# Kernel tuning notes

Measured on AMD Instinct MI355X. Metric: run time of the kernel, lower is better.

The kernel has to match this reference:

```python
import jax, jax.numpy as jnp
import numpy as np

N, IN_DIM, UNITS, Z_DEPTH, Z_K = 8192, 1024, 512, 32, 256


def setup_inputs() -> dict:
    key = jax.random.key(0)
    ks = jax.random.split(key, 10)
    s = 0.02
    return {
        "x": jax.random.normal(ks[0], (N, IN_DIM), jnp.float32),
        "h_W": jax.random.normal(ks[1], (IN_DIM, UNITS), jnp.float32) * s,
        "h_U": jax.random.normal(ks[2], (UNITS, UNITS), jnp.float32) * s,
        "h_b": jnp.zeros((UNITS,), jnp.float32),
        "f_W": jax.random.normal(ks[3], (UNITS, UNITS), jnp.float32) * s,
        "f_b": jnp.zeros((UNITS,), jnp.float32),
        "i_W": jax.random.normal(ks[4], (UNITS, UNITS), jnp.float32) * s,
        "i_b": jnp.zeros((UNITS,), jnp.float32),
        "c_W": jax.random.normal(ks[5], (UNITS, UNITS), jnp.float32) * s,
        "c_b": jnp.zeros((UNITS,), jnp.float32),
        "o_W": jax.random.normal(ks[6], (UNITS, UNITS), jnp.float32) * s,
        "o_b": jnp.zeros((UNITS,), jnp.float32),
        "t_W": jax.random.normal(ks[7], (UNITS, UNITS), jnp.float32) * s,
        "t_b": jnp.zeros((UNITS,), jnp.float32),
        "y_W": jax.random.normal(ks[8], (UNITS, Z_K), jnp.float32) * s,
        "y_b": jnp.zeros((Z_K,), jnp.float32),
        "h0": jnp.zeros((1, UNITS), jnp.float32),
        "z_depth": Z_DEPTH,
    }


def reference(x, h_W, h_U, h_b, f_W, f_b, i_W, i_b, c_W, c_b, o_W, o_b,
              t_W, t_b, y_W, y_b, h0, z_depth):
    n = x.shape[0]
    # x @ h_W is the same every step; hoist it out of the scan.
    xh = x @ h_W + h_b  # [n, units]

    def step(h_prev, _):
        h = jnp.tanh(xh + h_prev @ h_U)
        f = jax.nn.sigmoid(h @ f_W + f_b)
        i = jax.nn.sigmoid(h @ i_W + i_b)
        c = jnp.tanh(h @ c_W + c_b)
        o = jax.nn.sigmoid(h @ o_W + o_b)
        h1 = h_prev * f + c * i
        t = jnp.tanh((o * h1) @ t_W + t_b)
        y = jnp.tanh(t @ y_W + y_b)  # activation=tanh
        return h1, y

    h_init = jnp.broadcast_to(h0, (n, h0.shape[1]))
    _, ys = jax.lax.scan(step, h_init, None, length=z_depth)  # ys: [z_depth, n, z_k]
    return jnp.transpose(ys, (1, 0, 2))  # [n, z_depth, z_k]
```

## Files before the change

### kernel.cpp

```cpp
#include <hip/hip_runtime.h>


typedef _Float16 half_t;
typedef _Float16 half8 __attribute__((ext_vector_type(8)));
typedef _Float16 half4v __attribute__((ext_vector_type(4)));
typedef float float4_ __attribute__((ext_vector_type(4)));

#define UNITS 512
#define IN_DIM 1024
#define NROWS 8192
#define DEPTH 32
#define ZK 256
#define MT 32
#define PITCH (UNITS + 8)
#define XPITCH (IN_DIM + 8)

__device__ inline float4_ mfma16(half8 a, half8 b, float4_ c) {
  return __builtin_amdgcn_mfma_f32_16x16x32_f16(a, b, c, 0, 0, 0);
}
__device__ inline float fast_sigmoid(float x) {
  return __builtin_amdgcn_rcpf(1.0f + __builtin_amdgcn_exp2f(-1.4426950408889634f * x));
}
__device__ inline float fast_tanh(float x) {
  return 2.0f * __builtin_amdgcn_rcpf(1.0f + __builtin_amdgcn_exp2f(-2.8853900817779268f * x)) - 1.0f;
}

template<int NM, class OffF>
__device__ inline void sweepW(const half_t* __restrict__ wbase, OffF off,
                              const half_t* __restrict__ abase,
                              float4_ (&acc)[NM][2]) {
#pragma unroll
  for (int i = 0; i < NM; ++i) {
    acc[i][0] = {0.f, 0.f, 0.f, 0.f};
    acc[i][1] = {0.f, 0.f, 0.f, 0.f};
  }
  half8 w0[2][NM], w1[2][NM];
#pragma unroll
  for (int i = 0; i < NM; ++i) {
    w0[0][i] = *(const half8*)(wbase + off(i));
    w1[0][i] = *(const half8*)(wbase + off(i) + 32);
  }
#pragma unroll
  for (int kk = 0; kk < 8; ++kk) {
    const int cur = kk & 1, nxt = cur ^ 1;
    const int knext = ((kk + 1) & 7) * 64;
#pragma unroll
    for (int i = 0; i < NM; ++i) {
      w0[nxt][i] = *(const half8*)(wbase + off(i) + knext);
      w1[nxt][i] = *(const half8*)(wbase + off(i) + knext + 32);
    }
    const int k0 = kk * 64;
    half8 a00 = *(const half8*)(abase + k0);
    half8 a01 = *(const half8*)(abase + k0 + 32);
    half8 a10 = *(const half8*)(abase + 16 * PITCH + k0);
    half8 a11 = *(const half8*)(abase + 16 * PITCH + k0 + 32);
#pragma unroll
    for (int i = 0; i < NM; ++i) {
      acc[i][0] = mfma16(w0[cur][i], a00, acc[i][0]);
      acc[i][0] = mfma16(w1[cur][i], a01, acc[i][0]);
      acc[i][1] = mfma16(w0[cur][i], a10, acc[i][1]);
      acc[i][1] = mfma16(w1[cur][i], a11, acc[i][1]);
    }
  }
}

template<int NB, int K, int AP, class OffF>
__device__ inline void stage_gemm(const half_t* __restrict__ bbase, OffF off,
                                  const half_t* __restrict__ A, int q, int c16,
                                  float4_ (&acc)[NB][2]) {
#pragma unroll
  for (int nb = 0; nb < NB; ++nb) {
    acc[nb][0] = {0.f, 0.f, 0.f, 0.f};
    acc[nb][1] = {0.f, 0.f, 0.f, 0.f};
  }
  for (int k0 = 0; k0 < K; k0 += 64) {
    const half_t* ap = A + c16 * AP + k0 + q * 8;
    half8 a00 = *(const half8*)(ap);
    half8 a01 = *(const half8*)(ap + 32);
    half8 a10 = *(const half8*)(ap + 16 * AP);
    half8 a11 = *(const half8*)(ap + 16 * AP + 32);
#pragma unroll
    for (int nb = 0; nb < NB; ++nb) {
      const half_t* bp = bbase + off(nb) + k0;
      half8 b0 = *(const half8*)(bp);
      half8 b1 = *(const half8*)(bp + 32);
      acc[nb][0] = mfma16(a00, b0, acc[nb][0]);
      acc[nb][0] = mfma16(a01, b1, acc[nb][0]);
      acc[nb][1] = mfma16(a10, b0, acc[nb][1]);
      acc[nb][1] = mfma16(a11, b1, acc[nb][1]);
    }
  }
}

__global__ void transpose_convert(const float* __restrict__ in, half_t* __restrict__ out,
                                  int R, int C) {
  __shared__ float tile[32][33];
  int c0 = blockIdx.x * 32, r0 = blockIdx.y * 32;
  int tx = threadIdx.x, ty = threadIdx.y;
#pragma unroll
  for (int i = 0; i < 32; i += 8)
    tile[ty + i][tx] = in[(size_t)(r0 + ty + i) * C + c0 + tx];
  __syncthreads();
#pragma unroll
  for (int i = 0; i < 32; i += 8)
    out[(size_t)(c0 + ty + i) * R + r0 + tx] = (half_t)tile[tx][ty + i];
}

__global__ __launch_bounds__(512, 2) void xh_kernel(
    const float* __restrict__ x, const half_t* __restrict__ hW_T,
    const float* __restrict__ h_b, half_t* __restrict__ xh_g) {
  extern __shared__ half_t sx[];
  const int tid = threadIdx.x;
  const int w = tid >> 6, l = tid & 63, q = l >> 4, c16 = l & 15;
  const int row0 = blockIdx.x * 32;
  for (int it = tid; it < 32 * IN_DIM / 4; it += 512) {
    int r = it >> 8;
    int c = (it & 255) * 4;
    float4_ v = __builtin_nontemporal_load((const float4_*)(x + (size_t)(row0 + r) * IN_DIM + c));
    half4v hv;
    hv[0] = (half_t)v[0]; hv[1] = (half_t)v[1]; hv[2] = (half_t)v[2]; hv[3] = (half_t)v[3];
    *(half4v*)(sx + r * XPITCH + c) = hv;
  }
  __syncthreads();
  const int n0 = w * 64;
  float4_ acc[4][2];
  const half_t* bbase = hW_T + (size_t)(n0 + c16) * IN_DIM + q * 8;
  stage_gemm<4, IN_DIM, XPITCH>(bbase, [](int nb) { return nb * 16 * IN_DIM; }, sx, q, c16, acc);
#pragma unroll
  for (int nb = 0; nb < 4; ++nb)
#pragma unroll
    for (int mb = 0; mb < 2; ++mb)
#pragma unroll
      for (int r = 0; r < 4; ++r) {
        int row = mb * 16 + q * 4 + r;
        int col = n0 + nb * 16 + c16;
        xh_g[(size_t)(row0 + row) * UNITS + col] = (half_t)(acc[nb][mb][r] + h_b[col]);
      }
}

__global__ __launch_bounds__(512, 2) void lstm_main(
    const half_t* __restrict__ xh_g, const half_t* __restrict__ hU_T,
    const half_t* __restrict__ W4_T, const half_t* __restrict__ tW_T,
    const half_t* __restrict__ yW_T,
    const float* __restrict__ f_b, const float* __restrict__ i_b,
    const float* __restrict__ c_b, const float* __restrict__ o_b,
    const float* __restrict__ t_b, const float* __restrict__ y_b,
    const float* __restrict__ h0, float* __restrict__ out) {
  extern __shared__ half_t smem[];
  half_t* bufA = smem;
  half_t* bufB = smem + MT * PITCH;
  half_t* s_xh = smem + 2 * MT * PITCH;
  float* s_bias = (float*)(smem + 3 * MT * PITCH);
  float* s_fb = s_bias;
  float* s_ib = s_bias + 512;
  float* s_cb = s_bias + 1024;
  float* s_ob = s_bias + 1536;
  float* s_tb = s_bias + 2048;
  float* s_yb = s_bias + 2560;

  const int tid = threadIdx.x;
  const int w = tid >> 6, l = tid & 63, q = l >> 4, c16 = l & 15;
  const int row0 = blockIdx.x * MT;

  for (int it = tid; it < MT * UNITS / 8; it += 512) {
    int r = it >> 6;
    int c = (it & 63) * 8;
    float4_ v0 = *(const float4_*)(h0 + c);
    float4_ v1 = *(const float4_*)(h0 + c + 4);
    half8 hv;
#pragma unroll
    for (int j = 0; j < 4; ++j) { hv[j] = (half_t)v0[j]; hv[4 + j] = (half_t)v1[j]; }
    *(half8*)(bufA + r * PITCH + c) = hv;
    *(half8*)(s_xh + r * PITCH + c) = *(const half8*)(xh_g + (size_t)(row0 + r) * UNITS + c);
  }
  for (int it = tid; it < 512; it += 512) {
    s_fb[it] = f_b[it]; s_ib[it] = i_b[it]; s_cb[it] = c_b[it]; s_ob[it] = o_b[it];
    s_tb[it] = t_b[it];
    if (it < 256) s_yb[it] = y_b[it];
  }
  half4v state_r[2][2][2];
#pragma unroll
  for (int hh = 0; hh < 2; ++hh)
#pragma unroll
    for (int cm = 0; cm < 2; ++cm) {
      int col0 = hh * 256 + w * 32 + cm * 16 + q * 4;
      float4_ v = *(const float4_*)(h0 + col0);
      half4v s4;
#pragma unroll
      for (int r = 0; r < 4; ++r) s4[r] = (half_t)v[r];
#pragma unroll
      for (int rb = 0; rb < 2; ++rb) state_r[hh][cm][rb] = s4;
    }
  __syncthreads();

  const half_t* abase_off = (const half_t*)0 + c16 * PITCH + q * 8;
  (void)abase_off;

  for (int s = 0; s < DEPTH; ++s) {
    {
      float4_ acc[4][2];
      const half_t* wb = hU_T + (size_t)(w * 64 + c16) * UNITS + q * 8;
      sweepW<4>(wb, [](int i) { return i * 16 * UNITS; }, bufA + c16 * PITCH + q * 8, acc);
#pragma unroll
      for (int cm = 0; cm < 4; ++cm) {
        int col0 = w * 64 + cm * 16 + q * 4;
#pragma unroll
        for (int rb = 0; rb < 2; ++rb) {
          int row = rb * 16 + c16;
          half4v xh4 = *(const half4v*)(s_xh + row * PITCH + col0);
          half4v hv;
#pragma unroll
          for (int r = 0; r < 4; ++r) hv[r] = (half_t)fast_tanh(acc[cm][rb][r] + (float)xh4[r]);
          *(half4v*)(bufB + row * PITCH + col0) = hv;
        }
      }
    }
    __syncthreads();
#pragma unroll 1
    for (int hh = 0; hh < 2; ++hh) {
      float4_ acc[8][2];
      const int colbase = hh * 256 + w * 32;
      const half_t* wb = W4_T + (size_t)(colbase + c16) * UNITS + q * 8;
      sweepW<8>(wb, [](int i) { return (i >> 1) * (UNITS * UNITS) + (i & 1) * 16 * UNITS; },
                bufB + c16 * PITCH + q * 8, acc);
#pragma unroll
      for (int cm = 0; cm < 2; ++cm) {
        int col0 = colbase + cm * 16 + q * 4;
        float4_ fb4 = *(const float4_*)(s_fb + col0);
        float4_ ib4 = *(const float4_*)(s_ib + col0);
        float4_ cb4 = *(const float4_*)(s_cb + col0);
        float4_ ob4 = *(const float4_*)(s_ob + col0);
#pragma unroll
        for (int rb = 0; rb < 2; ++rb) {
          int row = rb * 16 + c16;
          half4v hp = state_r[hh][cm][rb];
          half4v h1v, sbv;
#pragma unroll
          for (int r = 0; r < 4; ++r) {
            float gf = fast_sigmoid(acc[0 * 2 + cm][rb][r] + fb4[r]);
            float gi = fast_sigmoid(acc[1 * 2 + cm][rb][r] + ib4[r]);
            float gc = fast_tanh   (acc[2 * 2 + cm][rb][r] + cb4[r]);
            float go = fast_sigmoid(acc[3 * 2 + cm][rb][r] + ob4[r]);
            float h1 = (float)hp[r] * gf + gc * gi;
            h1v[r] = (half_t)h1;
            sbv[r] = (half_t)(go * h1);
          }
          state_r[hh][cm][rb] = h1v;
          *(half4v*)(bufA + row * PITCH + col0) = sbv;
        }
      }
    }
    __syncthreads();
    {
      float4_ acc[4][2];
      const half_t* wb = tW_T + (size_t)(w * 64 + c16) * UNITS + q * 8;
      sweepW<4>(wb, [](int i) { return i * 16 * UNITS; }, bufA + c16 * PITCH + q * 8, acc);
#pragma unroll
      for (int cm = 0; cm < 4; ++cm) {
        int col0 = w * 64 + cm * 16 + q * 4;
        float4_ tb4 = *(const float4_*)(s_tb + col0);
#pragma unroll
        for (int rb = 0; rb < 2; ++rb) {
          int row = rb * 16 + c16;
          half4v hv;
#pragma unroll
          for (int r = 0; r < 4; ++r) hv[r] = (half_t)fast_tanh(acc[cm][rb][r] + tb4[r]);
          *(half4v*)(bufB + row * PITCH + col0) = hv;
        }
      }
    }
    __syncthreads();
    {
      float4_ acc[2][2];
      const half_t* wb = yW_T + (size_t)(w * 32 + c16) * UNITS + q * 8;
      sweepW<2>(wb, [](int i) { return i * 16 * UNITS; }, bufB + c16 * PITCH + q * 8, acc);
#pragma unroll
      for (int cm = 0; cm < 2; ++cm) {
        int col0 = w * 32 + cm * 16 + q * 4;
        float4_ yb4 = *(const float4_*)(s_yb + col0);
#pragma unroll
        for (int rb = 0; rb < 2; ++rb) {
          int row = rb * 16 + c16;
          float4_ yv;
#pragma unroll
          for (int r = 0; r < 4; ++r) yv[r] = fast_tanh(acc[cm][rb][r] + yb4[r]);
          __builtin_nontemporal_store(yv,
              (float4_*)(out + ((size_t)(row0 + row) * DEPTH + s) * ZK + col0));
        }
      }
#pragma unroll
      for (int hh = 0; hh < 2; ++hh)
#pragma unroll
        for (int cm = 0; cm < 2; ++cm) {
          int col0 = hh * 256 + w * 32 + cm * 16 + q * 4;
#pragma unroll
          for (int rb = 0; rb < 2; ++rb)
            *(half4v*)(bufA + (rb * 16 + c16) * PITCH + col0) = state_r[hh][cm][rb];
        }
    }
    __syncthreads();
  }
}

extern "C" void kernel_launch(void* const* d_in, const int* in_sizes, int n_in,
                              void* d_out, int out_size, void* d_ws, size_t ws_size,
                              hipStream_t stream) {
  (void)in_sizes; (void)n_in; (void)out_size; (void)ws_size;
  const float* x   = (const float*)d_in[0];
  const float* h_W = (const float*)d_in[1];
  const float* h_U = (const float*)d_in[2];
  const float* h_b = (const float*)d_in[3];
  const float* f_W = (const float*)d_in[4];
  const float* f_b = (const float*)d_in[5];
  const float* i_W = (const float*)d_in[6];
  const float* i_b = (const float*)d_in[7];
  const float* c_W = (const float*)d_in[8];
  const float* c_b = (const float*)d_in[9];
  const float* o_W = (const float*)d_in[10];
  const float* o_b = (const float*)d_in[11];
  const float* t_W = (const float*)d_in[12];
  const float* t_b = (const float*)d_in[13];
  const float* y_W = (const float*)d_in[14];
  const float* y_b = (const float*)d_in[15];
  const float* h0  = (const float*)d_in[16];
  float* out = (float*)d_out;

  half_t* ws   = (half_t*)d_ws;
  half_t* hW_T = ws;
  half_t* hU_T = hW_T + (size_t)UNITS * IN_DIM;
  half_t* W4_T = hU_T + (size_t)UNITS * UNITS;
  half_t* tW_T = W4_T + (size_t)4 * UNITS * UNITS;
  half_t* yW_T = tW_T + (size_t)UNITS * UNITS;
  half_t* xh_g = yW_T + (size_t)ZK * UNITS;

  const int lds_main = 3 * MT * PITCH * 2 + 2816 * 4;
  hipFuncSetAttribute((const void*)xh_kernel, hipFuncAttributeMaxDynamicSharedMemorySize,
                      32 * XPITCH * 2);
  hipFuncSetAttribute((const void*)lstm_main, hipFuncAttributeMaxDynamicSharedMemorySize,
                      lds_main);

  dim3 tb(32, 8);
  hipLaunchKernelGGL(transpose_convert, dim3(UNITS / 32, IN_DIM / 32), tb, 0, stream,
                     h_W, hW_T, IN_DIM, UNITS);
  hipLaunchKernelGGL(transpose_convert, dim3(UNITS / 32, UNITS / 32), tb, 0, stream,
                     h_U, hU_T, UNITS, UNITS);
  hipLaunchKernelGGL(transpose_convert, dim3(UNITS / 32, UNITS / 32), tb, 0, stream,
                     f_W, W4_T + 0 * (size_t)UNITS * UNITS, UNITS, UNITS);
  hipLaunchKernelGGL(transpose_convert, dim3(UNITS / 32, UNITS / 32), tb, 0, stream,
                     i_W, W4_T + 1 * (size_t)UNITS * UNITS, UNITS, UNITS);
  hipLaunchKernelGGL(transpose_convert, dim3(UNITS / 32, UNITS / 32), tb, 0, stream,
                     c_W, W4_T + 2 * (size_t)UNITS * UNITS, UNITS, UNITS);
  hipLaunchKernelGGL(transpose_convert, dim3(UNITS / 32, UNITS / 32), tb, 0, stream,
                     o_W, W4_T + 3 * (size_t)UNITS * UNITS, UNITS, UNITS);
  hipLaunchKernelGGL(transpose_convert, dim3(UNITS / 32, UNITS / 32), tb, 0, stream,
                     t_W, tW_T, UNITS, UNITS);
  hipLaunchKernelGGL(transpose_convert, dim3(ZK / 32, UNITS / 32), tb, 0, stream,
                     y_W, yW_T, UNITS, ZK);
  hipLaunchKernelGGL(xh_kernel, dim3(NROWS / 32), dim3(512), 32 * XPITCH * 2, stream,
                     x, hW_T, h_b, xh_g);
  hipLaunchKernelGGL(lstm_main, dim3(NROWS / MT), dim3(512), lds_main, stream,
                     xh_g, hU_T, W4_T, tW_T, yW_T, f_b, i_b, c_b, o_b, t_b, y_b, h0, out);
}
```

Baseline: 4.355 ms.

## Double block width to 1024 threads and stage outputs through LDS

The main LSTM kernel now runs 16 waves per block instead of 8, so each wave owns half as many output columns in every GEMM stage and the two-pass gate loop becomes a single pass. This cuts per-wave register pressure and gives more waves to hide latency. Final y values are also staged in shared memory and written out as coalesced rows instead of scattered per-lane global stores. The cost is extra LDS per block, one more copy pass per step, and launch bounds that assume 4 waves per SIMD, which may force register spills or limit blocks per CU.

Result: slower. 6.590 ms (+51.3%).

```diff
diff --git a/kernel.cpp b/kernel.cpp
--- a/kernel.cpp
+++ b/kernel.cpp
@@ -12,6 +12,7 @@
 #define DEPTH 32
 #define ZK 256
 #define MT 32
+#define NT 1024
 #define PITCH (UNITS + 8)
 #define XPITCH (IN_DIM + 8)
 
@@ -138,7 +139,7 @@
       }
 }
 
-__global__ __launch_bounds__(512, 2) void lstm_main(
+__global__ __launch_bounds__(NT, 4) void lstm_main(
     const half_t* __restrict__ xh_g, const half_t* __restrict__ hU_T,
     const half_t* __restrict__ W4_T, const half_t* __restrict__ tW_T,
     const half_t* __restrict__ yW_T,
@@ -157,12 +158,13 @@
   float* s_ob = s_bias + 1536;
   float* s_tb = s_bias + 2048;
   float* s_yb = s_bias + 2560;
+  float* s_y  = s_bias + 2816;
 
   const int tid = threadIdx.x;
   const int w = tid >> 6, l = tid & 63, q = l >> 4, c16 = l & 15;
   const int row0 = blockIdx.x * MT;
 
-  for (int it = tid; it < MT * UNITS / 8; it += 512) {
+  for (int it = tid; it < MT * UNITS / 8; it += NT) {
     int r = it >> 6;
     int c = (it & 63) * 8;
     float4_ v0 = *(const float4_*)(h0 + c);
@@ -173,37 +175,32 @@
     *(half8*)(bufA + r * PITCH + c) = hv;
     *(half8*)(s_xh + r * PITCH + c) = *(const half8*)(xh_g + (size_t)(row0 + r) * UNITS + c);
   }
-  for (int it = tid; it < 512; it += 512) {
-    s_fb[it] = f_b[it]; s_ib[it] = i_b[it]; s_cb[it] = c_b[it]; s_ob[it] = o_b[it];
-    s_tb[it] = t_b[it];
-    if (it < 256) s_yb[it] = y_b[it];
-  }
-  half4v state_r[2][2][2];
-#pragma unroll
-  for (int hh = 0; hh < 2; ++hh)
-#pragma unroll
-    for (int cm = 0; cm < 2; ++cm) {
-      int col0 = hh * 256 + w * 32 + cm * 16 + q * 4;
-      float4_ v = *(const float4_*)(h0 + col0);
-      half4v s4;
-#pragma unroll
-      for (int r = 0; r < 4; ++r) s4[r] = (half_t)v[r];
-#pragma unroll
-      for (int rb = 0; rb < 2; ++rb) state_r[hh][cm][rb] = s4;
-    }
+  if (tid < 512) {
+    s_fb[tid] = f_b[tid]; s_ib[tid] = i_b[tid]; s_cb[tid] = c_b[tid]; s_ob[tid] = o_b[tid];
+    s_tb[tid] = t_b[tid];
+    if (tid < 256) s_yb[tid] = y_b[tid];
+  }
+  half4v state_r[2][2];
+#pragma unroll
+  for (int cm = 0; cm < 2; ++cm) {
+    int col0 = w * 32 + cm * 16 + q * 4;
+    float4_ v = *(const float4_*)(h0 + col0);
+    half4v s4;
+#pragma unroll
+    for (int r = 0; r < 4; ++r) s4[r] = (half_t)v[r];
+    state_r[cm][0] = s4;
+    state_r[cm][1] = s4;
+  }
   __syncthreads();
-
-  const half_t* abase_off = (const half_t*)0 + c16 * PITCH + q * 8;
-  (void)abase_off;
 
   for (int s = 0; s < DEPTH; ++s) {
     {
-      float4_ acc[4][2];
-      const half_t* wb = hU_T + (size_t)(w * 64 + c16) * UNITS + q * 8;
-      sweepW<4>(wb, [](int i) { return i * 16 * UNITS; }, bufA + c16 * PITCH + q * 8, acc);
-#pragma unroll
-      for (int cm = 0; cm < 4; ++cm) {
-        int col0 = w * 64 + cm * 16 + q * 4;
+      float4_ acc[2][2];
+      const half_t* wb = hU_T + (size_t)(w * 32 + c16) * UNITS + q * 8;
+      sweepW<2>(wb, [](int i) { return i * 16 * UNITS; }, bufA + c16 * PITCH + q * 8, acc);
+#pragma unroll
+      for (int cm = 0; cm < 2; ++cm) {
+        int col0 = w * 32 + cm * 16 + q * 4;
 #pragma unroll
         for (int rb = 0; rb < 2; ++rb) {
           int row = rb * 16 + c16;
@@ -216,10 +213,9 @@
       }
     }
     __syncthreads();
-#pragma unroll 1
-    for (int hh = 0; hh < 2; ++hh) {
+    {
       float4_ acc[8][2];
-      const int colbase = hh * 256 + w * 32;
+      const int colbase = w * 32;
       const half_t* wb = W4_T + (size_t)(colbase + c16) * UNITS + q * 8;
       sweepW<8>(wb, [](int i) { return (i >> 1) * (UNITS * UNITS) + (i & 1) * 16 * UNITS; },
                 bufB + c16 * PITCH + q * 8, acc);
@@ -233,7 +229,7 @@
 #pragma unroll
         for (int rb = 0; rb < 2; ++rb) {
           int row = rb * 16 + c16;
-          half4v hp = state_r[hh][cm][rb];
+          half4v hp = state_r[cm][rb];
           half4v h1v, sbv;
 #pragma unroll
           for (int r = 0; r < 4; ++r) {
@@ -245,19 +241,19 @@
             h1v[r] = (half_t)h1;
             sbv[r] = (half_t)(go * h1);
           }
-          state_r[hh][cm][rb] = h1v;
+          state_r[cm][rb] = h1v;
           *(half4v*)(bufA + row * PITCH + col0) = sbv;
         }
       }
     }
     __syncthreads();
     {
-      float4_ acc[4][2];
-      const half_t* wb = tW_T + (size_t)(w * 64 + c16) * UNITS + q * 8;
-      sweepW<4>(wb, [](int i) { return i * 16 * UNITS; }, bufA + c16 * PITCH + q * 8, acc);
-#pragma unroll
-      for (int cm = 0; cm < 4; ++cm) {
-        int col0 = w * 64 + cm * 16 + q * 4;
+      float4_ acc[2][2];
+      const half_t* wb = tW_T + (size_t)(w * 32 + c16) * UNITS + q * 8;
+      sweepW<2>(wb, [](int i) { return i * 16 * UNITS; }, bufA + c16 * PITCH + q * 8, acc);
+#pragma unroll
+      for (int cm = 0; cm < 2; ++cm) {
+        int col0 = w * 32 + cm * 16 + q * 4;
         float4_ tb4 = *(const float4_*)(s_tb + col0);
 #pragma unroll
         for (int rb = 0; rb < 2; ++rb) {
@@ -271,34 +267,34 @@
     }
     __syncthreads();
     {
-      float4_ acc[2][2];
-      const half_t* wb = yW_T + (size_t)(w * 32 + c16) * UNITS + q * 8;
-      sweepW<2>(wb, [](int i) { return i * 16 * UNITS; }, bufB + c16 * PITCH + q * 8, acc);
+      float4_ acc[1][2];
+      const half_t* wb = yW_T + (size_t)(w * 16 + c16) * UNITS + q * 8;
+      sweepW<1>(wb, [](int i) { (void)i; return 0; }, bufB + c16 * PITCH + q * 8, acc);
+      const int col0 = w * 16 + q * 4;
+      float4_ yb4 = *(const float4_*)(s_yb + col0);
+#pragma unroll
+      for (int rb = 0; rb < 2; ++rb) {
+        int row = rb * 16 + c16;
+        float4_ yv;
+#pragma unroll
+        for (int r = 0; r < 4; ++r) yv[r] = fast_tanh(acc[0][rb][r] + yb4[r]);
+        *(float4_*)(s_y + row * ZK + col0) = yv;
+      }
 #pragma unroll
       for (int cm = 0; cm < 2; ++cm) {
-        int col0 = w * 32 + cm * 16 + q * 4;
-        float4_ yb4 = *(const float4_*)(s_yb + col0);
-#pragma unroll
-        for (int rb = 0; rb < 2; ++rb) {
-          int row = rb * 16 + c16;
-          float4_ yv;
-#pragma unroll
-          for (int r = 0; r < 4; ++r) yv[r] = fast_tanh(acc[cm][rb][r] + yb4[r]);
-          __builtin_nontemporal_store(yv,
-              (float4_*)(out + ((size_t)(row0 + row) * DEPTH + s) * ZK + col0));
-        }
-      }
-#pragma unroll
-      for (int hh = 0; hh < 2; ++hh)
-#pragma unroll
-        for (int cm = 0; cm < 2; ++cm) {
-          int col0 = hh * 256 + w * 32 + cm * 16 + q * 4;
-#pragma unroll
-          for (int rb = 0; rb < 2; ++rb)
-            *(half4v*)(bufA + (rb * 16 + c16) * PITCH + col0) = state_r[hh][cm][rb];
-        }
+        int sc0 = w * 32 + cm * 16 + q * 4;
+#pragma unroll
+        for (int rb = 0; rb < 2; ++rb)
+          *(half4v*)(bufA + (rb * 16 + c16) * PITCH + sc0) = state_r[cm][rb];
+      }
     }
     __syncthreads();
+    for (int it = tid; it < MT * ZK / 4; it += NT) {
+      int r = it >> 6;
+      int ch = (it & 63) * 4;
+      float4_ v = *(const float4_*)(s_y + r * ZK + ch);
+      __builtin_nontemporal_store(v, (float4_*)(out + ((size_t)(row0 + r) * DEPTH + s) * ZK + ch));
+    }
   }
 }
 
@@ -333,7 +329,7 @@
   half_t* yW_T = tW_T + (size_t)UNITS * UNITS;
   half_t* xh_g = yW_T + (size_t)ZK * UNITS;
 
-  const int lds_main = 3 * MT * PITCH * 2 + 2816 * 4;
+  const int lds_main = 3 * MT * PITCH * 2 + 2816 * 4 + MT * ZK * 4;
   hipFuncSetAttribute((const void*)xh_kernel, hipFuncAttributeMaxDynamicSharedMemorySize,
                       32 * XPITCH * 2);
   hipFuncSetAttribute((const void*)lstm_main, hipFuncAttributeMaxDynamicSharedMemorySize,
@@ -358,6 +354,6 @@
                      y_W, yW_T, UNITS, ZK);
   hipLaunchKernelGGL(xh_kernel, dim3(NROWS / 32), dim3(512), 32 * XPITCH * 2, stream,
                      x, hW_T, h_b, xh_g);
-  hipLaunchKernelGGL(lstm_main, dim3(NROWS / MT), dim3(512), lds_main, stream,
+  hipLaunchKernelGGL(lstm_main, dim3(NROWS / MT), dim3(NT), lds_main, stream,
                      xh_g, hU_T, W4_T, tW_T, yW_T, f_b, i_b, c_b, o_b, t_b, y_b, h0, out);
 }
```

## Halve row tile to 16 and stage y output through LDS for coalesced stores

Applied to the files above, without the earlier changes.

Shrinks the per-block row tile from 32 to 16, doubling the grid to 512 blocks and halving accumulator registers, but each block now re-streams all weights from global/L2 for half as many rows. The y outputs are staged into a new LDS buffer and then written with coalesced float4 nontemporal stores instead of scattered per-lane stores. The aim is higher occupancy and better store coalescing, at the cost of twice the weight traffic per output row.

Result: slower. 7.600 ms (+74.5%).

```diff
diff --git a/kernel.cpp b/kernel.cpp
--- a/kernel.cpp
+++ b/kernel.cpp
@@ -11,7 +11,7 @@
 #define NROWS 8192
 #define DEPTH 32
 #define ZK 256
-#define MT 32
+#define MT 16
 #define PITCH (UNITS + 8)
 #define XPITCH (IN_DIM + 8)
 
@@ -28,12 +28,9 @@
 template<int NM, class OffF>
 __device__ inline void sweepW(const half_t* __restrict__ wbase, OffF off,
                               const half_t* __restrict__ abase,
-                              float4_ (&acc)[NM][2]) {
-#pragma unroll
-  for (int i = 0; i < NM; ++i) {
-    acc[i][0] = {0.f, 0.f, 0.f, 0.f};
-    acc[i][1] = {0.f, 0.f, 0.f, 0.f};
-  }
+                              float4_ (&acc)[NM]) {
+#pragma unroll
+  for (int i = 0; i < NM; ++i) acc[i] = {0.f, 0.f, 0.f, 0.f};
   half8 w0[2][NM], w1[2][NM];
 #pragma unroll
   for (int i = 0; i < NM; ++i) {
@@ -50,16 +47,12 @@
       w1[nxt][i] = *(const half8*)(wbase + off(i) + knext + 32);
     }
     const int k0 = kk * 64;
-    half8 a00 = *(const half8*)(abase + k0);
-    half8 a01 = *(const half8*)(abase + k0 + 32);
-    half8 a10 = *(const half8*)(abase + 16 * PITCH + k0);
-    half8 a11 = *(const half8*)(abase + 16 * PITCH + k0 + 32);
+    half8 a0 = *(const half8*)(abase + k0);
+    half8 a1 = *(const half8*)(abase + k0 + 32);
 #pragma unroll
     for (int i = 0; i < NM; ++i) {
-      acc[i][0] = mfma16(w0[cur][i], a00, acc[i][0]);
-      acc[i][0] = mfma16(w1[cur][i], a01, acc[i][0]);
-      acc[i][1] = mfma16(w0[cur][i], a10, acc[i][1]);
-      acc[i][1] = mfma16(w1[cur][i], a11, acc[i][1]);
+      acc[i] = mfma16(w0[cur][i], a0, acc[i]);
+      acc[i] = mfma16(w1[cur][i], a1, acc[i]);
     }
   }
 }
@@ -157,6 +150,7 @@
   float* s_ob = s_bias + 1536;
   float* s_tb = s_bias + 2048;
   float* s_yb = s_bias + 2560;
+  float* s_y  = s_bias + 2816;
 
   const int tid = threadIdx.x;
   const int w = tid >> 6, l = tid & 63, q = l >> 4, c16 = l & 15;
@@ -173,12 +167,12 @@
     *(half8*)(bufA + r * PITCH + c) = hv;
     *(half8*)(s_xh + r * PITCH + c) = *(const half8*)(xh_g + (size_t)(row0 + r) * UNITS + c);
   }
-  for (int it = tid; it < 512; it += 512) {
-    s_fb[it] = f_b[it]; s_ib[it] = i_b[it]; s_cb[it] = c_b[it]; s_ob[it] = o_b[it];
-    s_tb[it] = t_b[it];
-    if (it < 256) s_yb[it] = y_b[it];
-  }
-  half4v state_r[2][2][2];
+  if (tid < 512) {
+    s_fb[tid] = f_b[tid]; s_ib[tid] = i_b[tid]; s_cb[tid] = c_b[tid]; s_ob[tid] = o_b[tid];
+    s_tb[tid] = t_b[tid];
+    if (tid < 256) s_yb[tid] = y_b[tid];
+  }
+  half4v state_r[2][2];
 #pragma unroll
   for (int hh = 0; hh < 2; ++hh)
 #pragma unroll
@@ -188,37 +182,29 @@
       half4v s4;
 #pragma unroll
       for (int r = 0; r < 4; ++r) s4[r] = (half_t)v[r];
-#pragma unroll
-      for (int rb = 0; rb < 2; ++rb) state_r[hh][cm][rb] = s4;
+      state_r[hh][cm] = s4;
     }
   __syncthreads();
-
-  const half_t* abase_off = (const half_t*)0 + c16 * PITCH + q * 8;
-  (void)abase_off;
 
   for (int s = 0; s < DEPTH; ++s) {
     {
-      float4_ acc[4][2];
+      float4_ acc[4];
       const half_t* wb = hU_T + (size_t)(w * 64 + c16) * UNITS + q * 8;
       sweepW<4>(wb, [](int i) { return i * 16 * UNITS; }, bufA + c16 * PITCH + q * 8, acc);
 #pragma unroll
       for (int cm = 0; cm < 4; ++cm) {
         int col0 = w * 64 + cm * 16 + q * 4;
-#pragma unroll
-        for (int rb = 0; rb < 2; ++rb) {
-          int row = rb * 16 + c16;
-          half4v xh4 = *(const half4v*)(s_xh + row * PITCH + col0);
-          half4v hv;
-#pragma unroll
-          for (int r = 0; r < 4; ++r) hv[r] = (half_t)fast_tanh(acc[cm][rb][r] + (float)xh4[r]);
-          *(half4v*)(bufB + row * PITCH + col0) = hv;
-        }
+        half4v xh4 = *(const half4v*)(s_xh + c16 * PITCH + col0);
+        half4v hv;
+#pragma unroll
+        for (int r = 0; r < 4; ++r) hv[r] = (half_t)fast_tanh(acc[cm][r] + (float)xh4[r]);
+        *(half4v*)(bufB + c16 * PITCH + col0) = hv;
       }
     }
     __syncthreads();
 #pragma unroll 1
     for (int hh = 0; hh < 2; ++hh) {
-      float4_ acc[8][2];
+      float4_ acc[8];
       const int colbase = hh * 256 + w * 32;
       const half_t* wb = W4_T + (size_t)(colbase + c16) * UNITS + q * 8;
       sweepW<8>(wb, [](int i) { return (i >> 1) * (UNITS * UNITS) + (i & 1) * 16 * UNITS; },
@@ -230,75 +216,66 @@
         float4_ ib4 = *(const float4_*)(s_ib + col0);
         float4_ cb4 = *(const float4_*)(s_cb + col0);
         float4_ ob4 = *(const float4_*)(s_ob + col0);
-#pragma unroll
-        for (int rb = 0; rb < 2; ++rb) {
-          int row = rb * 16 + c16;
-          half4v hp = state_r[hh][cm][rb];
-          half4v h1v, sbv;
-#pragma unroll
-          for (int r = 0; r < 4; ++r) {
-            float gf = fast_sigmoid(acc[0 * 2 + cm][rb][r] + fb4[r]);
-            float gi = fast_sigmoid(acc[1 * 2 + cm][rb][r] + ib4[r]);
-            float gc = fast_tanh   (acc[2 * 2 + cm][rb][r] + cb4[r]);
-            float go = fast_sigmoid(acc[3 * 2 + cm][rb][r] + ob4[r]);
-            float h1 = (float)hp[r] * gf + gc * gi;
-            h1v[r] = (half_t)h1;
-            sbv[r] = (half_t)(go * h1);
-          }
-          state_r[hh][cm][rb] = h1v;
-          *(half4v*)(bufA + row * PITCH + col0) = sbv;
+        half4v hp = state_r[hh][cm];
+        half4v h1v, sbv;
+#pragma unroll
+        for (int r = 0; r < 4; ++r) {
+          float gf = fast_sigmoid(acc[0 * 2 + cm][r] + fb4[r]);
+          float gi = fast_sigmoid(acc[1 * 2 + cm][r] + ib4[r]);
+          float gc = fast_tanh   (acc[2 * 2 + cm][r] + cb4[r]);
+          float go = fast_sigmoid(acc[3 * 2 + cm][r] + ob4[r]);
+          float h1 = (float)hp[r] * gf + gc * gi;
+          h1v[r] = (half_t)h1;
+          sbv[r] = (half_t)(go * h1);
         }
+        state_r[hh][cm] = h1v;
+        *(half4v*)(bufA + c16 * PITCH + col0) = sbv;
       }
     }
     __syncthreads();
     {
-      float4_ acc[4][2];
+      float4_ acc[4];
       const half_t* wb = tW_T + (size_t)(w * 64 + c16) * UNITS + q * 8;
       sweepW<4>(wb, [](int i) { return i * 16 * UNITS; }, bufA + c16 * PITCH + q * 8, acc);
 #pragma unroll
       for (int cm = 0; cm < 4; ++cm) {
         int col0 = w * 64 + cm * 16 + q * 4;
         float4_ tb4 = *(const float4_*)(s_tb + col0);
-#pragma unroll
-        for (int rb = 0; rb < 2; ++rb) {
-          int row = rb * 16 + c16;
-          half4v hv;
-#pragma unroll
-          for (int r = 0; r < 4; ++r) hv[r] = (half_t)fast_tanh(acc[cm][rb][r] + tb4[r]);
-          *(half4v*)(bufB + row * PITCH + col0) = hv;
-        }
+        half4v hv;
+#pragma unroll
+        for (int r = 0; r < 4; ++r) hv[r] = (half_t)fast_tanh(acc[cm][r] + tb4[r]);
+        *(half4v*)(bufB + c16 * PITCH + col0) = hv;
       }
     }
     __syncthreads();
     {
-      float4_ acc[2][2];
+      float4_ acc[2];
       const half_t* wb = yW_T + (size_t)(w * 32 + c16) * UNITS + q * 8;
       sweepW<2>(wb, [](int i) { return i * 16 * UNITS; }, bufB + c16 * PITCH + q * 8, acc);
 #pragma unroll
       for (int cm = 0; cm < 2; ++cm) {
-        int col0 = w * 32 + cm * 16 + q * 4;
+        const int col0 = w * 32 + cm * 16 + q * 4;
         float4_ yb4 = *(const float4_*)(s_yb + col0);
-#pragma unroll
-        for (int rb = 0; rb < 2; ++rb) {
-          int row = rb * 16 + c16;
-          float4_ yv;
-#pragma unroll
-          for (int r = 0; r < 4; ++r) yv[r] = fast_tanh(acc[cm][rb][r] + yb4[r]);
-          __builtin_nontemporal_store(yv,
-              (float4_*)(out + ((size_t)(row0 + row) * DEPTH + s) * ZK + col0));
+        float4_ yv;
+#pragma unroll
+        for (int r = 0; r < 4; ++r) yv[r] = fast_tanh(acc[cm][r] + yb4[r]);
+        *(float4_*)(s_y + c16 * ZK + col0) = yv;
+      }
+#pragma unroll
+      for (int hh = 0; hh < 2; ++hh)
+#pragma unroll
+        for (int cm = 0; cm < 2; ++cm) {
+          int sc0 = hh * 256 + w * 32 + cm * 16 + q * 4;
+          *(half4v*)(bufA + c16 * PITCH + sc0) = state_r[hh][cm];
         }
-      }
-#pragma unroll
-      for (int hh = 0; hh < 2; ++hh)
-#pragma unroll
-        for (int cm = 0; cm < 2; ++cm) {
-          int col0 = hh * 256 + w * 32 + cm * 16 + q * 4;
-#pragma unroll
-          for (int rb = 0; rb < 2; ++rb)
-            *(half4v*)(bufA + (rb * 16 + c16) * PITCH + col0) = state_r[hh][cm][rb];
-        }
     }
     __syncthreads();
+    for (int it = tid; it < MT * ZK / 4; it += 512) {
+      int r = it >> 6;
+      int ch = (it & 63) * 4;
+      float4_ v = *(const float4_*)(s_y + r * ZK + ch);
+      __builtin_nontemporal_store(v, (float4_*)(out + ((size_t)(row0 + r) * DEPTH + s) * ZK + ch));
+    }
   }
 }
 
@@ -333,7 +310,7 @@
   half_t* yW_T = tW_T + (size_t)UNITS * UNITS;
   half_t* xh_g = yW_T + (size_t)ZK * UNITS;
 
-  const int lds_main = 3 * MT * PITCH * 2 + 2816 * 4;
+  const int lds_main = 3 * MT * PITCH * 2 + 2816 * 4 + MT * ZK * 4;
   hipFuncSetAttribute((const void*)xh_kernel, hipFuncAttributeMaxDynamicSharedMemorySize,
                       32 * XPITCH * 2);
   hipFuncSetAttribute((const void*)lstm_main, hipFuncAttributeMaxDynamicSharedMemorySize,
```
